# Kernel tuning notes

Hardware: AMD Instinct MI355X
Metric: run time of the kernel (lower is better)

## Reference

```python
import jax, jax.numpy as jnp
import numpy as np

N_NODES = 100000
N_EDGES = 1000000
N_GRAPHS = 5000
H = 64
F_IN = 14  # QM9 num_features (11) + pos (3)
BN_EPS = 1e-5


def setup_inputs() -> dict:
    key = jax.random.key(0)
    ks = jax.random.split(key, 16)

    def w(k, shape, fan_in):
        return (jax.random.normal(k, shape, jnp.float32) / np.sqrt(fan_in)).astype(jnp.float32)

    inp = {
        "x": jax.random.normal(ks[0], (N_NODES, 11), jnp.float32),
        "pos": jax.random.normal(ks[1], (N_NODES, 3), jnp.float32),
        "edge_index": jax.random.randint(ks[2], (2, N_EDGES), 0, N_NODES, dtype=jnp.int32),
        "batch": jnp.sort(jax.random.randint(ks[3], (N_NODES,), 0, N_GRAPHS, dtype=jnp.int32)),
    }
    dims = [F_IN, H, H]
    i = 4
    for l, din in enumerate(dims, 1):
        inp[f"w{l}a"] = w(ks[i], (din, H), din); i += 1
        inp[f"b{l}a"] = jnp.zeros((H,), jnp.float32)
        inp[f"g{l}"] = jnp.ones((H,), jnp.float32)   # BatchNorm gamma
        inp[f"be{l}"] = jnp.zeros((H,), jnp.float32)  # BatchNorm beta
        inp[f"w{l}b"] = w(ks[i], (H, H), H); i += 1
        inp[f"b{l}b"] = jnp.zeros((H,), jnp.float32)
    inp["wl1"] = w(ks[i], (3 * H, H), 3 * H); i += 1
    inp["bl1"] = jnp.zeros((H,), jnp.float32)
    inp["wl2"] = w(ks[i], (H, 1), H)
    inp["bl2"] = jnp.zeros((1,), jnp.float32)
    return inp


def _gin_layer(x, src, dst, w1, b1, g, be, w2, b2):
    # GINConv (eps=0): h = MLP(x + sum_{j in N(i)} x_j)
    agg = jax.ops.segment_sum(x[src], dst, num_segments=x.shape[0])
    h = (x + agg) @ w1 + b1
    # BatchNorm1d in training mode: batch stats over node dim (biased var)
    mu = jnp.mean(h, axis=0)
    var = jnp.mean((h - mu) ** 2, axis=0)
    h = jax.nn.relu(g * (h - mu) * jax.lax.rsqrt(var + BN_EPS) + be)
    return jax.nn.relu(h @ w2 + b2)


def _mean_pool(x, batch):
    s = jax.ops.segment_sum(x, batch, num_segments=N_GRAPHS)
    c = jax.ops.segment_sum(jnp.ones((x.shape[0], 1), x.dtype), batch, num_segments=N_GRAPHS)
    return s / jnp.maximum(c, 1.0)


def reference(x, pos, edge_index, batch,
              w1a, b1a, g1, be1, w1b, b1b,
              w2a, b2a, g2, be2, w2b, b2b,
              w3a, b3a, g3, be3, w3b, b3b,
              wl1, bl1, wl2, bl2):
    src, dst = edge_index[0], edge_index[1]
    h0 = jnp.concatenate([x, pos], axis=1)                 # [N, 14]
    x1 = _gin_layer(h0, src, dst, w1a, b1a, g1, be1, w1b, b1b)
    x2 = _gin_layer(x1, src, dst, w2a, b2a, g2, be2, w2b, b2b)
    x3 = _gin_layer(x2, src, dst, w3a, b3a, g3, be3, w3b, b3b)
    p = jnp.concatenate([_mean_pool(x1, batch), _mean_pool(x2, batch), _mean_pool(x3, batch)], axis=1)  # [G, 192]
    h = jax.nn.relu(p @ wl1 + bl1)
    return h @ wl2 + bl2                                   # [G, 1]
```

## Files before the change

### kernel.cpp

```cpp
#include <hip/hip_runtime.h>
#include <hip/hip_bf16.h>

#define BN_EPS 1e-5f
#define LDP 132
#define LDS_BF 72
#define BSH 9
#define EPB 4096

typedef short bf16x8 __attribute__((ext_vector_type(8)));
typedef float f32x4 __attribute__((ext_vector_type(4)));

__device__ __forceinline__ float loadf(const void* p, long long i, unsigned bf) {
    if (bf) return __bfloat162float(((const __hip_bfloat16*)p)[i]);
    return ((const float*)p)[i];
}
__device__ __forceinline__ float b2f(unsigned short u) {
    return __uint_as_float(((unsigned)u) << 16);
}
__device__ __forceinline__ unsigned short f2b(float f) {
    __hip_bfloat16 h = __float2bfloat16(f);
    return *(unsigned short*)&h;
}
__device__ __forceinline__ float blo(unsigned u) { return __uint_as_float(u << 16); }
__device__ __forceinline__ float bhi(unsigned u) { return __uint_as_float(u & 0xffff0000u); }
__device__ __forceinline__ unsigned bfflag(const unsigned* g1w) {
    return (*g1w == 0x3F803F80u) ? 1u : 0u;
}

struct Srcs { const void* p[22]; };

__global__ __launch_bounds__(256) void k_prep(Srcs s, const unsigned* g1w, float* dst, unsigned short* wbt,
                                              const void* x, const void* pos, const int* batch,
                                              unsigned short* h0b, float* cnt, int N) {
    unsigned bf = bfflag(g1w);
    int t = blockIdx.x;
    if (t < 22) {
        const int sizes[22] = {896,64,64,64,4096,64,  4096,64,64,64,4096,64,
                               4096,64,64,64,4096,64, 12288,64,64,1};
        const int offs[22]  = {0,896,960,1024,1088,5184, 5248,9344,9408,9472,9536,13632,
                               13696,17792,17856,17920,17984,22080, 22144,34432,34496,34560};
        const void* src = s.p[t];
        float* d = dst + offs[t];
        int n = sizes[t];
        for (int i = threadIdx.x; i < n; i += blockDim.x) d[i] = loadf(src, i, bf);
    } else if (t < 27) {
        const int widx[5] = {4, 6, 10, 12, 16};
        const void* src = s.p[widx[t - 22]];
        unsigned short* dw = wbt + (t - 22) * 4096;
        for (int i = threadIdx.x; i < 4096; i += blockDim.x) {
            int n = i >> 6, k = i & 63;
            dw[n * 64 + k] = f2b(loadf(src, (long long)k * 64 + n, bf));
        }
    } else {
        int i = (t - 27) * 256 + threadIdx.x;
        if (i >= N) return;
        unsigned short v[16];
        #pragma unroll
        for (int k = 0; k < 11; k++) v[k] = f2b(loadf(x, (long long)i * 11 + k, bf));
        #pragma unroll
        for (int k = 0; k < 3; k++) v[11 + k] = f2b(loadf(pos, (long long)i * 3 + k, bf));
        v[14] = 0; v[15] = 0;
        #pragma unroll
        for (int k = 0; k < 4; k++)
            *(ushort4*)&h0b[(long long)i * 16 + k * 4] = make_ushort4(v[4*k], v[4*k+1], v[4*k+2], v[4*k+3]);
        atomicAdd(&cnt[batch[i]], 1.0f);
    }
}

__global__ __launch_bounds__(256) void k_bhist(const int* __restrict__ ei, int* __restrict__ bcnt,
                                               int* __restrict__ bktot, int E, int NCH, int NBK) {
    __shared__ int h[1024];
    int c = blockIdx.x, t = threadIdx.x;
    for (int i = t; i < NBK; i += 256) h[i] = 0;
    __syncthreads();
    int base = c * EPB;
    for (int i = t; i < EPB; i += 256) {
        int e = base + i;
        if (e < E) atomicAdd(&h[ei[E + e] >> BSH], 1);
    }
    __syncthreads();
    for (int i = t; i < NBK; i += 256) {
        bcnt[i * NCH + c] = h[i];
        if (h[i]) atomicAdd(&bktot[i], h[i]);
    }
}

__global__ __launch_bounds__(256) void k_scan_all(const int* __restrict__ bcnt, const int* __restrict__ bktot,
                                                  int* __restrict__ boff, int NCH, int NBK) {
    __shared__ int sp[256];
    __shared__ int sS;
    int b = blockIdx.x, t = threadIdx.x;
    int v = (t < NBK) ? bktot[t] : 0;
    sp[t] = v;
    __syncthreads();
    for (int off = 1; off < 256; off <<= 1) {
        int u = (t >= off) ? sp[t - off] : 0;
        __syncthreads();
        sp[t] += u;
        __syncthreads();
    }
    if (t == 0) sS = (b == 0) ? 0 : sp[b - 1];
    __syncthreads();
    int running = sS;
    for (int base = 0; base < NCH; base += 256) {
        int c = base + t;
        int val = (c < NCH) ? bcnt[b * NCH + c] : 0;
        __syncthreads();
        sp[t] = val;
        __syncthreads();
        for (int off = 1; off < 256; off <<= 1) {
            int u = (t >= off) ? sp[t - off] : 0;
            __syncthreads();
            sp[t] += u;
            __syncthreads();
        }
        if (c < NCH) boff[b * NCH + c] = running + sp[t] - val;
        running += sp[255];
    }
}

__global__ __launch_bounds__(256) void k_place(const int* __restrict__ ei, const int* __restrict__ boff,
                                               unsigned* __restrict__ ebuf, int E, int NCH, int NBK) {
    __shared__ int cur[1024];
    int c = blockIdx.x, t = threadIdx.x;
    for (int i = t; i < NBK; i += 256) cur[i] = boff[i * NCH + c];
    __syncthreads();
    int base = c * EPB;
    for (int i = t; i < EPB; i += 256) {
        int e = base + i;
        if (e < E) {
            int s = ei[e], d = ei[E + e];
            int pos = atomicAdd(&cur[d >> BSH], 1);
            ebuf[pos] = ((unsigned)(d & 511) << 23) | (unsigned)s;
        }
    }
}

__global__ __launch_bounds__(256) void k_bucket_fill(const unsigned* __restrict__ ebuf, const int* __restrict__ boff,
                                                     int* __restrict__ roff, int* __restrict__ csr,
                                                     int N, int E, int NCH, int NBK) {
    __shared__ int cnt[512];
    __shared__ int exc[512];
    __shared__ int curb[512];
    __shared__ int sp[256];
    int b = blockIdx.x, t = threadIdx.x;
    int d0 = b << BSH;
    int dpb = N - d0; if (dpb > 512) dpb = 512;
    int segS = boff[b * NCH];
    int segE = (b + 1 < NBK) ? boff[(b + 1) * NCH] : E;
    cnt[t] = 0; cnt[t + 256] = 0;
    __syncthreads();
    for (int k = segS + t; k < segE; k += 256) atomicAdd(&cnt[ebuf[k] >> 23], 1);
    __syncthreads();
    int a0 = cnt[2 * t], a1 = cnt[2 * t + 1];
    sp[t] = a0 + a1;
    __syncthreads();
    for (int off = 1; off < 256; off <<= 1) {
        int v = (t >= off) ? sp[t - off] : 0;
        __syncthreads();
        sp[t] += v;
        __syncthreads();
    }
    int pre = (t == 0) ? 0 : sp[t - 1];
    exc[2 * t] = pre; exc[2 * t + 1] = pre + a0;
    curb[2 * t] = pre; curb[2 * t + 1] = pre + a0;
    __syncthreads();
    for (int i = t; i < dpb; i += 256) roff[d0 + i] = segS + exc[i];
    if (b == NBK - 1 && t == 0) roff[N] = E;
    for (int k = segS + t; k < segE; k += 256) {
        unsigned p = ebuf[k];
        int lp = atomicAdd(&curb[p >> 23], 1);
        csr[segS + lp] = (int)(p & 0x7FFFFFu);
    }
}

__global__ __launch_bounds__(256) void k_gather14b(const int* __restrict__ roff, const int* __restrict__ csr,
                                                   const unsigned short* __restrict__ h0b,
                                                   unsigned short* __restrict__ aggb, int N) {
    int q = threadIdx.x & 7, nn = threadIdx.x >> 3;
    int node = blockIdx.x * 32 + nn;
    if (node >= N) return;
    const unsigned* h0u = (const unsigned*)h0b;
    unsigned su = h0u[(long long)node * 8 + q];
    float a0 = blo(su), a1 = bhi(su);
    float b0 = 0.f, b1 = 0.f, c0 = 0.f, c1 = 0.f, d0 = 0.f, d1 = 0.f;
    int e0 = roff[node], e1 = roff[node + 1];
    int k = e0;
    for (; k + 3 < e1; k += 4) {
        unsigned u0 = h0u[(long long)csr[k] * 8 + q];
        unsigned u1 = h0u[(long long)csr[k + 1] * 8 + q];
        unsigned u2 = h0u[(long long)csr[k + 2] * 8 + q];
        unsigned u3 = h0u[(long long)csr[k + 3] * 8 + q];
        a0 += blo(u0); a1 += bhi(u0);
        b0 += blo(u1); b1 += bhi(u1);
        c0 += blo(u2); c1 += bhi(u2);
        d0 += blo(u3); d1 += bhi(u3);
    }
    for (; k < e1; k++) {
        unsigned u0 = h0u[(long long)csr[k] * 8 + q];
        a0 += blo(u0); a1 += bhi(u0);
    }
    a0 += b0 + c0 + d0; a1 += b1 + c1 + d1;
    unsigned outw = (unsigned)f2b(a0) | ((unsigned)f2b(a1) << 16);
    ((unsigned*)aggb)[(long long)node * 8 + q] = outw;
}

__global__ __launch_bounds__(256) void k_mm_bn14b(const unsigned short* __restrict__ aggb,
        const float* __restrict__ W, const float* __restrict__ bias, unsigned short* __restrict__ Hb,
        float* bnsum, float* bnsumsq, int N) {
    __shared__ float sA[14 * LDP];
    __shared__ float sW[14 * 64];
    __shared__ float sRs[4 * 64];
    __shared__ float sRq[4 * 64];
    int tid = threadIdx.x;
    int row0 = blockIdx.x * 128;
    int rows = N - row0; if (rows > 128) rows = 128;
    for (int i = tid; i < 14 * 64; i += 256) sW[i] = W[i];
    const unsigned* au = (const unsigned*)aggb;
    #pragma unroll
    for (int it = 0; it < 4; it++) {
        int idx = tid + it * 256;
        int r = idx >> 3, q = idx & 7;
        unsigned u = (r < rows) ? au[(long long)(row0 + r) * 8 + q] : 0u;
        if (2 * q < 14)     sA[(2 * q) * LDP + r] = blo(u);
        if (2 * q + 1 < 14) sA[(2 * q + 1) * LDP + r] = bhi(u);
    }
    __syncthreads();
    int tx = tid & 15, ty = tid >> 4;
    float4 bj = *(const float4*)&bias[tx * 4];
    float acc[8][4];
    #pragma unroll
    for (int i = 0; i < 8; i++) { acc[i][0] = bj.x; acc[i][1] = bj.y; acc[i][2] = bj.z; acc[i][3] = bj.w; }
    #pragma unroll
    for (int k = 0; k < 14; k++) {
        const float4 a0 = *(const float4*)&sA[k * LDP + ty * 8];
        const float4 a1 = *(const float4*)&sA[k * LDP + ty * 8 + 4];
        const float4 w  = *(const float4*)&sW[k * 64 + tx * 4];
        const float av[8] = {a0.x, a0.y, a0.z, a0.w, a1.x, a1.y, a1.z, a1.w};
        #pragma unroll
        for (int i = 0; i < 8; i++) {
            acc[i][0] += av[i] * w.x; acc[i][1] += av[i] * w.y;
            acc[i][2] += av[i] * w.z; acc[i][3] += av[i] * w.w;
        }
    }
    float cs[4] = {0.f, 0.f, 0.f, 0.f}, cq[4] = {0.f, 0.f, 0.f, 0.f};
    #pragma unroll
    for (int i = 0; i < 8; i++) {
        int r = ty * 8 + i;
        if (r < rows) {
            int gr = row0 + r;
            ushort4 hv;
            hv.x = f2b(acc[i][0]); hv.y = f2b(acc[i][1]);
            hv.z = f2b(acc[i][2]); hv.w = f2b(acc[i][3]);
            *(ushort4*)&Hb[(long long)gr * 64 + tx * 4] = hv;
            #pragma unroll
            for (int d = 0; d < 4; d++) { cs[d] += acc[i][d]; cq[d] += acc[i][d] * acc[i][d]; }
        }
    }
    #pragma unroll
    for (int d = 0; d < 4; d++) {
        cs[d] += __shfl_xor(cs[d], 16); cs[d] += __shfl_xor(cs[d], 32);
        cq[d] += __shfl_xor(cq[d], 16); cq[d] += __shfl_xor(cq[d], 32);
    }
    int wid = tid >> 6, lane = tid & 63;
    if (lane < 16) {
        #pragma unroll
        for (int d = 0; d < 4; d++) {
            sRs[wid * 64 + lane * 4 + d] = cs[d];
            sRq[wid * 64 + lane * 4 + d] = cq[d];
        }
    }
    __syncthreads();
    if (tid < 64) atomicAdd(&bnsum[tid], sRs[tid] + sRs[64 + tid] + sRs[128 + tid] + sRs[192 + tid]);
    else if (tid < 128) {
        int j = tid - 64;
        atomicAdd(&bnsumsq[j], sRq[j] + sRq[64 + j] + sRq[128 + j] + sRq[192 + j]);
    }
}

__global__ __launch_bounds__(256) void k_gather64(const int* __restrict__ roff, const int* __restrict__ csr,
                                                  const unsigned short* __restrict__ xinb,
                                                  unsigned short* __restrict__ aggb, int N) {
    int g = threadIdx.x >> 4, q = threadIdx.x & 15;
    int node = blockIdx.x * 16 + g;
    if (node >= N) return;
    const ushort4* xr = (const ushort4*)xinb;
    ushort4 u = xr[(long long)node * 16 + q];
    float4 a0 = make_float4(b2f(u.x), b2f(u.y), b2f(u.z), b2f(u.w));
    float4 a1 = make_float4(0.f, 0.f, 0.f, 0.f);
    float4 a2 = make_float4(0.f, 0.f, 0.f, 0.f);
    float4 a3 = make_float4(0.f, 0.f, 0.f, 0.f);
    int e0 = roff[node], e1 = roff[node + 1];
    int k = e0;
    for (; k + 3 < e1; k += 4) {
        int s0 = csr[k], s1 = csr[k + 1], s2 = csr[k + 2], s3 = csr[k + 3];
        ushort4 v0 = xr[(long long)s0 * 16 + q];
        ushort4 v1 = xr[(long long)s1 * 16 + q];
        ushort4 v2 = xr[(long long)s2 * 16 + q];
        ushort4 v3 = xr[(long long)s3 * 16 + q];
        a0.x += b2f(v0.x); a0.y += b2f(v0.y); a0.z += b2f(v0.z); a0.w += b2f(v0.w);
        a1.x += b2f(v1.x); a1.y += b2f(v1.y); a1.z += b2f(v1.z); a1.w += b2f(v1.w);
        a2.x += b2f(v2.x); a2.y += b2f(v2.y); a2.z += b2f(v2.z); a2.w += b2f(v2.w);
        a3.x += b2f(v3.x); a3.y += b2f(v3.y); a3.z += b2f(v3.z); a3.w += b2f(v3.w);
    }
    for (; k < e1; k++) {
        ushort4 v0 = xr[(long long)csr[k] * 16 + q];
        a0.x += b2f(v0.x); a0.y += b2f(v0.y); a0.z += b2f(v0.z); a0.w += b2f(v0.w);
    }
    a0.x += a1.x + a2.x + a3.x;
    a0.y += a1.y + a2.y + a3.y;
    a0.z += a1.z + a2.z + a3.z;
    a0.w += a1.w + a2.w + a3.w;
    ushort4 o;
    o.x = f2b(a0.x); o.y = f2b(a0.y); o.z = f2b(a0.z); o.w = f2b(a0.w);
    *(ushort4*)&aggb[(long long)node * 64 + q * 4] = o;
}

__global__ __launch_bounds__(256) void k_mm_bn64(const unsigned short* __restrict__ Sb,
        const unsigned short* __restrict__ Wt,
        const float* __restrict__ bias, unsigned short* __restrict__ Hb,
        float* bnsum, float* bnsumsq, int N) {
    __shared__ unsigned short sS[128 * LDS_BF];
    __shared__ unsigned short sWt[64 * LDS_BF];
    __shared__ float sRs[4 * 64];
    __shared__ float sRq[4 * 64];
    int tid = threadIdx.x;
    int row0 = blockIdx.x * 128;
    int rows = N - row0; if (rows > 128) rows = 128;
    #pragma unroll
    for (int it = 0; it < 8; it++) {
        int idx = tid + it * 256;
        int r = idx >> 4, q = idx & 15;
        ushort4 v = make_ushort4(0, 0, 0, 0);
        if (r < rows) v = *(const ushort4*)&Sb[(long long)(row0 + r) * 64 + (q << 2)];
        *(ushort4*)&sS[r * LDS_BF + q * 4] = v;
    }
    #pragma unroll
    for (int it = 0; it < 4; it++) {
        int i = tid + it * 256;
        ushort4 v = ((const ushort4*)Wt)[i];
        int n = i >> 4, k4 = (i & 15) << 2;
        *(ushort4*)&sWt[n * LDS_BF + k4] = v;
    }
    __syncthreads();
    int w = tid >> 6, lane = tid & 63;
    int half = lane >> 4, m = lane & 15;
    f32x4 acc[2][4];
    #pragma unroll
    for (int rt = 0; rt < 2; rt++)
        #pragma unroll
        for (int ct = 0; ct < 4; ct++) acc[rt][ct] = (f32x4){0.f, 0.f, 0.f, 0.f};
    #pragma unroll
    for (int km = 0; km < 2; km++) {
        bf16x8 a0 = *(const bf16x8*)&sS[(w * 32 + m) * LDS_BF + km * 32 + half * 8];
        bf16x8 a1 = *(const bf16x8*)&sS[(w * 32 + 16 + m) * LDS_BF + km * 32 + half * 8];
        #pragma unroll
        for (int ct = 0; ct < 4; ct++) {
            bf16x8 b = *(const bf16x8*)&sWt[(ct * 16 + m) * LDS_BF + km * 32 + half * 8];
            acc[0][ct] = __builtin_amdgcn_mfma_f32_16x16x32_bf16(a0, b, acc[0][ct], 0, 0, 0);
            acc[1][ct] = __builtin_amdgcn_mfma_f32_16x16x32_bf16(a1, b, acc[1][ct], 0, 0, 0);
        }
    }
    float cs[4] = {0.f, 0.f, 0.f, 0.f}, cq[4] = {0.f, 0.f, 0.f, 0.f};
    #pragma unroll
    for (int ct = 0; ct < 4; ct++) {
        float bj = bias[ct * 16 + m];
        #pragma unroll
        for (int rt = 0; rt < 2; rt++) {
            #pragma unroll
            for (int r = 0; r < 4; r++) {
                int lr = w * 32 + rt * 16 + half * 4 + r;
                if (lr < rows) {
                    float v = acc[rt][ct][r] + bj;
                    Hb[(long long)(row0 + lr) * 64 + ct * 16 + m] = f2b(v);
                    cs[ct] += v; cq[ct] += v * v;
                }
            }
        }
    }
    #pragma unroll
    for (int d = 0; d < 4; d++) {
        cs[d] += __shfl_xor(cs[d], 16); cs[d] += __shfl_xor(cs[d], 32);
        cq[d] += __shfl_xor(cq[d], 16); cq[d] += __shfl_xor(cq[d], 32);
    }
    if (lane < 16) {
        #pragma unroll
        for (int ct = 0; ct < 4; ct++) {
            sRs[w * 64 + ct * 16 + lane] = cs[ct];
            sRq[w * 64 + ct * 16 + lane] = cq[ct];
        }
    }
    __syncthreads();
    if (tid < 64) atomicAdd(&bnsum[tid], sRs[tid] + sRs[64 + tid] + sRs[128 + tid] + sRs[192 + tid]);
    else if (tid < 128) {
        int j = tid - 64;
        atomicAdd(&bnsumsq[j], sRq[j] + sRq[64 + j] + sRq[128 + j] + sRq[192 + j]);
    }
}

__global__ __launch_bounds__(256) void k_bn_mm2_rt(const unsigned short* __restrict__ Hb, const float* __restrict__ g,
        const float* __restrict__ be, const unsigned short* __restrict__ Wt, const float* __restrict__ b2,
        const float* bnsum, const float* bnsumsq, const int* __restrict__ batch,
        unsigned short* __restrict__ xout, float* pool, int N, float invN, int loff) {
    __shared__ unsigned short sS[128 * LDS_BF];
    __shared__ unsigned short sWt[64 * LDS_BF];
    __shared__ float sSc[64];
    __shared__ float sSh[64];
    int tid = threadIdx.x;
    int row0 = blockIdx.x * 128;
    int rows = N - row0; if (rows > 128) rows = 128;
    if (tid < 64) {
        float mu = bnsum[tid] * invN;
        float var = bnsumsq[tid] * invN - mu * mu;
        float sc = g[tid] * rsqrtf(var + BN_EPS);
        sSc[tid] = sc; sSh[tid] = be[tid] - sc * mu;
    }
    #pragma unroll
    for (int it = 0; it < 4; it++) {
        int i = tid + it * 256;
        ushort4 v = ((const ushort4*)Wt)[i];
        int n = i >> 4, k4 = (i & 15) << 2;
        *(ushort4*)&sWt[n * LDS_BF + k4] = v;
    }
    __syncthreads();
    #pragma unroll
    for (int it = 0; it < 8; it++) {
        int idx = tid + it * 256;
        int r = idx >> 4, q = idx & 15;
        ushort4 o = make_ushort4(0, 0, 0, 0);
        if (r < rows) {
            ushort4 u = *(const ushort4*)&Hb[(long long)(row0 + r) * 64 + (q << 2)];
            o.x = f2b(fmaxf(sSc[q*4+0] * b2f(u.x) + sSh[q*4+0], 0.f));
            o.y = f2b(fmaxf(sSc[q*4+1] * b2f(u.y) + sSh[q*4+1], 0.f));
            o.z = f2b(fmaxf(sSc[q*4+2] * b2f(u.z) + sSh[q*4+2], 0.f));
            o.w = f2b(fmaxf(sSc[q*4+3] * b2f(u.w) + sSh[q*4+3], 0.f));
        }
        *(ushort4*)&sS[r * LDS_BF + q * 4] = o;
    }
    __syncthreads();
    int w = tid >> 6, lane = tid & 63;
    int half = lane >> 4, m = lane & 15;
    f32x4 acc[2][4];
    #pragma unroll
    for (int rt = 0; rt < 2; rt++)
        #pragma unroll
        for (int ct = 0; ct < 4; ct++) acc[rt][ct] = (f32x4){0.f, 0.f, 0.f, 0.f};
    #pragma unroll
    for (int km = 0; km < 2; km++) {
        bf16x8 a0 = *(const bf16x8*)&sS[(w * 32 + m) * LDS_BF + km * 32 + half * 8];
        bf16x8 a1 = *(const bf16x8*)&sS[(w * 32 + 16 + m) * LDS_BF + km * 32 + half * 8];
        #pragma unroll
        for (int ct = 0; ct < 4; ct++) {
            bf16x8 b = *(const bf16x8*)&sWt[(ct * 16 + m) * LDS_BF + km * 32 + half * 8];
            acc[0][ct] = __builtin_amdgcn_mfma_f32_16x16x32_bf16(a0, b, acc[0][ct], 0, 0, 0);
            acc[1][ct] = __builtin_amdgcn_mfma_f32_16x16x32_bf16(a1, b, acc[1][ct], 0, 0, 0);
        }
    }
    float b2j[4];
    #pragma unroll
    for (int ct = 0; ct < 4; ct++) b2j[ct] = b2[ct * 16 + m];
    int prevg = -1;
    float p[4] = {0.f, 0.f, 0.f, 0.f};
    #pragma unroll
    for (int rt = 0; rt < 2; rt++) {
        #pragma unroll
        for (int r = 0; r < 4; r++) {
            int lr = w * 32 + rt * 16 + half * 4 + r;
            if (lr < rows) {
                int gr = row0 + lr;
                float o[4];
                #pragma unroll
                for (int ct = 0; ct < 4; ct++) {
                    o[ct] = fmaxf(acc[rt][ct][r] + b2j[ct], 0.f);
                    if (xout) xout[(long long)gr * 64 + ct * 16 + m] = f2b(o[ct]);
                }
                int gid = batch[gr];
                if (gid != prevg) {
                    if (prevg >= 0) {
                        float* pp = &pool[(long long)prevg * 192 + loff + m];
                        atomicAdd(pp + 0,  p[0]); atomicAdd(pp + 16, p[1]);
                        atomicAdd(pp + 32, p[2]); atomicAdd(pp + 48, p[3]);
                    }
                    prevg = gid;
                    p[0] = o[0]; p[1] = o[1]; p[2] = o[2]; p[3] = o[3];
                } else {
                    p[0] += o[0]; p[1] += o[1]; p[2] += o[2]; p[3] += o[3];
                }
            }
        }
    }
    if (prevg >= 0) {
        float* pp = &pool[(long long)prevg * 192 + loff + m];
        atomicAdd(pp + 0,  p[0]); atomicAdd(pp + 16, p[1]);
        atomicAdd(pp + 32, p[2]); atomicAdd(pp + 48, p[3]);
    }
}

__global__ __launch_bounds__(64) void k_head(const float* pool, const float* cnt,
                        const float* wl1, const float* bl1, const float* wl2, const float* bl2,
                        const unsigned* g1w, void* out, int G) {
    int gb = blockIdx.x; int j = threadIdx.x;
    if (gb >= G) return;
    __shared__ float sP[192];
    float c = fmaxf(cnt[gb], 1.0f);
    float inv = 1.0f / c;
    for (int k = j; k < 192; k += 64) sP[k] = pool[(long long)gb * 192 + k] * inv;
    __syncthreads();
    float acc = bl1[j];
    for (int k = 0; k < 192; k++) acc += sP[k] * wl1[k * 64 + j];
    float v = fmaxf(acc, 0.f) * wl2[j];
    #pragma unroll
    for (int off = 32; off; off >>= 1) v += __shfl_down(v, off);
    if (j == 0) {
        float res = v + bl2[0];
        if (bfflag(g1w)) ((__hip_bfloat16*)out)[gb] = __float2bfloat16(res);
        else             ((float*)out)[gb] = res;
    }
}

extern "C" void kernel_launch(void* const* d_in, const int* in_sizes, int n_in,
                              void* d_out, int out_size, void* d_ws, size_t ws_size,
                              hipStream_t stream) {
    const void* x   = d_in[0];
    const void* pos = d_in[1];
    const int* ei    = (const int*)d_in[2];
    const int* batch = (const int*)d_in[3];
    const unsigned* g1w = (const unsigned*)d_in[6];
    const int N = in_sizes[3];
    const int E = in_sizes[2] / 2;
    const int G = out_size;

    float* ws = (float*)d_ws;
    float* P = ws + 16;
    float* w1a = P + 0;     float* b1a = P + 896;   float* g1 = P + 960;   float* be1 = P + 1024;
    float* b1b = P + 5184;
    float* b2a = P + 9344;  float* g2 = P + 9408;  float* be2 = P + 9472;
    float* b2b = P + 13632;
    float* b3a = P + 17792; float* g3 = P + 17856; float* be3 = P + 17920;
    float* b3b = P + 22080;
    float* wl1 = P + 22144; float* bl1 = P + 34432; float* wl2 = P + 34496; float* bl2 = P + 34560;

    long long off = 16 + 34592;
    unsigned short* wbt = (unsigned short*)(ws + off);  off += 10240;
    float* h0r  = ws + off;                 off += (long long)N * 14;
    float* aggr = ws + off;                 off += (long long)N * 64;
    float* Hbuf = ws + off;                 off += (long long)N * 64;
    float* curf = ws + off;                 off += (long long)N * 64;
    float* pool = ws + off;                 off += (long long)G * 192;
    float* cnt  = ws + off;                 off += G;
    float* bn   = ws + off;                 off += 384;
    int* bktot  = (int*)(ws + off);         off += 256;
    int*   roff = (int*)(ws + off);
    int* csr = roff + (N + 1);

    unsigned short* h0b  = (unsigned short*)h0r;
    unsigned short* aggh = (unsigned short*)aggr;
    unsigned short* curh = (unsigned short*)curf;
    unsigned short* Hh   = (unsigned short*)Hbuf;
    unsigned short* w1bT = wbt + 0 * 4096;
    unsigned short* w2aT = wbt + 1 * 4096;
    unsigned short* w2bT = wbt + 2 * 4096;
    unsigned short* w3aT = wbt + 3 * 4096;
    unsigned short* w3bT = wbt + 4 * 4096;

    const int NBK = (N + 511) >> BSH;
    const int NCH = (E + EPB - 1) / EPB;
    const int M = NBK * NCH;
    int* bcnt     = csr + E;
    int* boff     = bcnt + M;
    unsigned* ebuf = (unsigned*)Hbuf;

    hipMemsetAsync(pool, 0, ((size_t)G * 192 + (size_t)G + 384 + 256) * sizeof(float), stream);

    Srcs s;
    for (int i = 0; i < 22; i++) s.p[i] = d_in[4 + i];
    int nb = (N + 255) / 256;
    k_prep<<<27 + nb, 256, 0, stream>>>(s, g1w, P, wbt, x, pos, batch, h0b, cnt, N);

    k_bhist<<<NCH, 256, 0, stream>>>(ei, bcnt, bktot, E, NCH, NBK);
    k_scan_all<<<NBK, 256, 0, stream>>>(bcnt, bktot, boff, NCH, NBK);
    k_place<<<NCH, 256, 0, stream>>>(ei, boff, ebuf, E, NCH, NBK);
    k_bucket_fill<<<NBK, 256, 0, stream>>>(ebuf, boff, roff, csr, N, E, NCH, NBK);

    int rtBlocks = (N + 127) / 128;
    int gBlocks = (N + 15) / 16;
    int g14Blocks = (N + 31) / 32;
    float invN = 1.0f / (float)N;
    float* bn1 = bn;
    float* bn2 = bn + 128;
    float* bn3 = bn + 256;

    k_gather14b<<<g14Blocks, 256, 0, stream>>>(roff, csr, h0b, aggh, N);
    k_mm_bn14b<<<rtBlocks, 256, 0, stream>>>(aggh, w1a, b1a, Hh, bn1, bn1 + 64, N);
    k_bn_mm2_rt<<<rtBlocks, 256, 0, stream>>>(Hh, g1, be1, w1bT, b1b, bn1, bn1 + 64, batch,
                                              curh, pool, N, invN, 0);
    k_gather64<<<gBlocks, 256, 0, stream>>>(roff, csr, curh, aggh, N);
    k_mm_bn64<<<rtBlocks, 256, 0, stream>>>(aggh, w2aT, b2a, Hh, bn2, bn2 + 64, N);
    k_bn_mm2_rt<<<rtBlocks, 256, 0, stream>>>(Hh, g2, be2, w2bT, b2b, bn2, bn2 + 64, batch,
                                              curh, pool, N, invN, 64);
    k_gather64<<<gBlocks, 256, 0, stream>>>(roff, csr, curh, aggh, N);
    k_mm_bn64<<<rtBlocks, 256, 0, stream>>>(aggh, w3aT, b3a, Hh, bn3, bn3 + 64, N);
    k_bn_mm2_rt<<<rtBlocks, 256, 0, stream>>>(Hh, g3, be3, w3bT, b3b, bn3, bn3 + 64, batch,
                                              nullptr, pool, N, invN, 128);

    k_head<<<G, 64, 0, stream>>>(pool, cnt, wl1, bl1, wl2, bl2, g1w, d_out, G);
}
```

Before: 342.0 us.

## Fuse histogram and zeroing into prep kernel, derive graph counts by binary search

Merges the edge bucket histogram and the pool/BN buffer zeroing into the prep kernel as extra block ranges, which removes a memset and a separate launch. The per-bucket totals and their atomics go away: each scan block now sums all preceding bucket counts itself. Per-graph node counts are no longer built with atomics; the head kernel binary-searches the sorted batch array instead and applies 1/count after the matvec. This cuts launches and atomics at the cost of redundant prefix reads in the scan and a reliance on batch being sorted.

```diff
diff --git a/kernel.cpp b/kernel.cpp
--- a/kernel.cpp
+++ b/kernel.cpp
@@ -6,6 +6,7 @@
 #define LDS_BF 72
 #define BSH 9
 #define EPB 4096
+#define ZB 64
 
 typedef short bf16x8 __attribute__((ext_vector_type(8)));
 typedef float f32x4 __attribute__((ext_vector_type(4)));
@@ -30,8 +31,11 @@
 struct Srcs { const void* p[22]; };
 
 __global__ __launch_bounds__(256) void k_prep(Srcs s, const unsigned* g1w, float* dst, unsigned short* wbt,
-                                              const void* x, const void* pos, const int* batch,
-                                              unsigned short* h0b, float* cnt, int N) {
+                                              const void* x, const void* pos,
+                                              unsigned short* h0b, int N,
+                                              const int* ei, int* bcnt, int E, int NCH, int NBK,
+                                              float* zbase, int nzero4, int nb) {
+    __shared__ int h[1024];
     unsigned bf = bfflag(g1w);
     int t = blockIdx.x;
     if (t < 22) {
@@ -51,7 +55,7 @@
             int n = i >> 6, k = i & 63;
             dw[n * 64 + k] = f2b(loadf(src, (long long)k * 64 + n, bf));
         }
-    } else {
+    } else if (t < 27 + nb) {
         int i = (t - 27) * 256 + threadIdx.x;
         if (i >= N) return;
         unsigned short v[16];
@@ -63,43 +67,40 @@
         #pragma unroll
         for (int k = 0; k < 4; k++)
             *(ushort4*)&h0b[(long long)i * 16 + k * 4] = make_ushort4(v[4*k], v[4*k+1], v[4*k+2], v[4*k+3]);
-        atomicAdd(&cnt[batch[i]], 1.0f);
-    }
-}
-
-__global__ __launch_bounds__(256) void k_bhist(const int* __restrict__ ei, int* __restrict__ bcnt,
-                                               int* __restrict__ bktot, int E, int NCH, int NBK) {
-    __shared__ int h[1024];
-    int c = blockIdx.x, t = threadIdx.x;
-    for (int i = t; i < NBK; i += 256) h[i] = 0;
-    __syncthreads();
-    int base = c * EPB;
-    for (int i = t; i < EPB; i += 256) {
-        int e = base + i;
-        if (e < E) atomicAdd(&h[ei[E + e] >> BSH], 1);
-    }
-    __syncthreads();
-    for (int i = t; i < NBK; i += 256) {
-        bcnt[i * NCH + c] = h[i];
-        if (h[i]) atomicAdd(&bktot[i], h[i]);
-    }
-}
-
-__global__ __launch_bounds__(256) void k_scan_all(const int* __restrict__ bcnt, const int* __restrict__ bktot,
+    } else if (t < 27 + nb + NCH) {
+        int c = t - 27 - nb;
+        int tid = threadIdx.x;
+        for (int i = tid; i < NBK; i += 256) h[i] = 0;
+        __syncthreads();
+        int base = c * EPB;
+        for (int i = tid; i < EPB; i += 256) {
+            int e = base + i;
+            if (e < E) atomicAdd(&h[ei[E + e] >> BSH], 1);
+        }
+        __syncthreads();
+        for (int i = tid; i < NBK; i += 256) bcnt[i * NCH + c] = h[i];
+    } else {
+        int z = t - 27 - nb - NCH;
+        float4 zero = make_float4(0.f, 0.f, 0.f, 0.f);
+        for (int i = z * 256 + threadIdx.x; i < nzero4; i += ZB * 256)
+            ((float4*)zbase)[i] = zero;
+    }
+}
+
+__global__ __launch_bounds__(256) void k_scan_all(const int* __restrict__ bcnt,
                                                   int* __restrict__ boff, int NCH, int NBK) {
     __shared__ int sp[256];
+    __shared__ int swv[4];
     __shared__ int sS;
     int b = blockIdx.x, t = threadIdx.x;
-    int v = (t < NBK) ? bktot[t] : 0;
-    sp[t] = v;
-    __syncthreads();
-    for (int off = 1; off < 256; off <<= 1) {
-        int u = (t >= off) ? sp[t - off] : 0;
-        __syncthreads();
-        sp[t] += u;
-        __syncthreads();
-    }
-    if (t == 0) sS = (b == 0) ? 0 : sp[b - 1];
+    int partial = 0;
+    int pref = b * NCH;
+    for (int i = t; i < pref; i += 256) partial += bcnt[i];
+    #pragma unroll
+    for (int o = 32; o; o >>= 1) partial += __shfl_down(partial, o);
+    if ((t & 63) == 0) swv[t >> 6] = partial;
+    __syncthreads();
+    if (t == 0) sS = swv[0] + swv[1] + swv[2] + swv[3];
     __syncthreads();
     int running = sS;
     for (int base = 0; base < NCH; base += 256) {
@@ -496,19 +497,29 @@
     }
 }
 
-__global__ __launch_bounds__(64) void k_head(const float* pool, const float* cnt,
+__global__ __launch_bounds__(64) void k_head(const float* pool, const int* __restrict__ batch, int N,
                         const float* wl1, const float* bl1, const float* wl2, const float* bl2,
                         const unsigned* g1w, void* out, int G) {
     int gb = blockIdx.x; int j = threadIdx.x;
     if (gb >= G) return;
     __shared__ float sP[192];
-    float c = fmaxf(cnt[gb], 1.0f);
-    float inv = 1.0f / c;
-    for (int k = j; k < 192; k += 64) sP[k] = pool[(long long)gb * 192 + k] * inv;
-    __syncthreads();
-    float acc = bl1[j];
+    __shared__ int sLB, sUB;
+    if (j == 0) {
+        int lo = 0, hi = N;
+        while (lo < hi) { int mid = (lo + hi) >> 1; if (batch[mid] < gb) lo = mid + 1; else hi = mid; }
+        sLB = lo;
+    }
+    if (j == 1) {
+        int lo = 0, hi = N;
+        while (lo < hi) { int mid = (lo + hi) >> 1; if (batch[mid] <= gb) lo = mid + 1; else hi = mid; }
+        sUB = lo;
+    }
+    for (int k = j; k < 192; k += 64) sP[k] = pool[(long long)gb * 192 + k];
+    __syncthreads();
+    float inv = 1.0f / fmaxf((float)(sUB - sLB), 1.0f);
+    float acc = 0.f;
     for (int k = 0; k < 192; k++) acc += sP[k] * wl1[k * 64 + j];
-    float v = fmaxf(acc, 0.f) * wl2[j];
+    float v = fmaxf(acc * inv + bl1[j], 0.f) * wl2[j];
     #pragma unroll
     for (int off = 32; off; off >>= 1) v += __shfl_down(v, off);
     if (j == 0) {
@@ -547,9 +558,7 @@
     float* Hbuf = ws + off;                 off += (long long)N * 64;
     float* curf = ws + off;                 off += (long long)N * 64;
     float* pool = ws + off;                 off += (long long)G * 192;
-    float* cnt  = ws + off;                 off += G;
     float* bn   = ws + off;                 off += 384;
-    int* bktot  = (int*)(ws + off);         off += 256;
     int*   roff = (int*)(ws + off);
     int* csr = roff + (N + 1);
 
@@ -570,15 +579,15 @@
     int* boff     = bcnt + M;
     unsigned* ebuf = (unsigned*)Hbuf;
 
-    hipMemsetAsync(pool, 0, ((size_t)G * 192 + (size_t)G + 384 + 256) * sizeof(float), stream);
+    int nzero4 = (G * 192 + 384) / 4;
 
     Srcs s;
     for (int i = 0; i < 22; i++) s.p[i] = d_in[4 + i];
     int nb = (N + 255) / 256;
-    k_prep<<<27 + nb, 256, 0, stream>>>(s, g1w, P, wbt, x, pos, batch, h0b, cnt, N);
-
-    k_bhist<<<NCH, 256, 0, stream>>>(ei, bcnt, bktot, E, NCH, NBK);
-    k_scan_all<<<NBK, 256, 0, stream>>>(bcnt, bktot, boff, NCH, NBK);
+    k_prep<<<27 + nb + NCH + ZB, 256, 0, stream>>>(s, g1w, P, wbt, x, pos, h0b, N,
+                                                   ei, bcnt, E, NCH, NBK, pool, nzero4, nb);
+
+    k_scan_all<<<NBK, 256, 0, stream>>>(bcnt, boff, NCH, NBK);
     k_place<<<NCH, 256, 0, stream>>>(ei, boff, ebuf, E, NCH, NBK);
     k_bucket_fill<<<NBK, 256, 0, stream>>>(ebuf, boff, roff, csr, N, E, NCH, NBK);
 
@@ -603,5 +612,5 @@
     k_bn_mm2_rt<<<rtBlocks, 256, 0, stream>>>(Hh, g3, be3, w3bT, b3b, bn3, bn3 + 64, batch,
                                               nullptr, pool, N, invN, 128);
 
-    k_head<<<G, 64, 0, stream>>>(pool, cnt, wl1, bl1, wl2, bl2, g1w, d_out, G);
-}
+    k_head<<<G, 64, 0, stream>>>(pool, batch, N, wl1, bl1, wl2, bl2, g1w, d_out, G);
+}
```

Result: faster. 327.8 us, median of 2 (-4.1%).
